# Kernel tuning notes

Hardware: AMD Instinct MI355X
Metric: run time of the kernel (lower is better)

The kernel has to match this reference:

```python
import jax, jax.numpy as jnp
import numpy as np

B = 1024        # graphs per batch
NPG = 64        # nodes per graph (uniform)
DEG = 16        # avg degree
NE_PG = 256     # candidate non-edges per graph
N = B * NPG
E = N * DEG
NE = B * NE_PG
EMB, HID, NCAT, NET, NOUT = 64, 128, 100, 4, 101  # NOUT = num_external + 1


def setup_inputs() -> dict:
    key = jax.random.key(0)
    ks = jax.random.split(key, 32)
    rn = lambda k, shape: jax.random.normal(k, shape, jnp.float32) * 0.05
    # graph structure: edges and non-edges stay within each graph's node block
    x = jax.random.randint(ks[0], (N,), 0, NCAT)
    offs = jnp.repeat(jnp.arange(B) * NPG, NPG * DEG)
    src = jax.random.randint(ks[1], (E,), 0, NPG) + offs
    dst = jax.random.randint(ks[2], (E,), 0, NPG) + offs
    edge_index = jnp.stack([src, dst])
    edge_attr = jax.random.randint(ks[3], (E,), 0, NET)
    offs_ne = jnp.repeat(jnp.arange(B) * NPG, NE_PG)
    non_edges = jax.random.randint(ks[4], (NE, 2), 0, NPG) + offs_ne[:, None]
    batch = jnp.repeat(jnp.arange(B), NPG)
    return dict(
        node_tab=rn(ks[5], (NCAT, EMB)), edge_tab=rn(ks[6], (NET, EMB)),
        c1_w=rn(ks[7], (EMB, HID)), c1_we=rn(ks[8], (EMB, HID)),
        c1_as=rn(ks[9], (HID,)), c1_ad=rn(ks[10], (HID,)), c1_ae=rn(ks[11], (HID,)), c1_b=rn(ks[12], (HID,)),
        c2_w=rn(ks[13], (HID, HID)), c2_we=rn(ks[14], (EMB, HID)),
        c2_as=rn(ks[15], (HID,)), c2_ad=rn(ks[16], (HID,)), c2_ae=rn(ks[17], (HID,)), c2_b=rn(ks[18], (HID,)),
        s_w1=rn(ks[19], (HID, HID)), s_b1=rn(ks[20], (HID,)), s_w2=rn(ks[21], (HID, 1)), s_b2=rn(ks[22], (1,)),
        n_w1=rn(ks[23], (HID, HID)), n_b1=rn(ks[24], (HID,)), n_w2=rn(ks[25], (HID, NOUT)), n_b2=rn(ks[26], (NOUT,)),
        e_w1=rn(ks[27], (HID, HID)), e_b1=rn(ks[28], (HID,)), e_w2=rn(ks[29], (HID, 1)), e_b2=rn(ks[30], (1,)),
        x=x, edge_index=edge_index, edge_attr=edge_attr, non_edges=non_edges, batch=batch,
    )


def _gat(h_in, src, dst, e, W, We, a_s, a_d, a_e, b):
    """PyG GATConv, heads=1: gather -> leakyrelu logits -> segment softmax over dst -> scatter sum."""
    n = h_in.shape[0]
    h = h_in @ W                  # [N, C]
    he = e @ We                   # [E, C]
    logit = (h @ a_s)[src] + (h @ a_d)[dst] + he @ a_e   # [E]
    logit = jnp.where(logit > 0, logit, 0.2 * logit)      # leaky_relu(0.2)
    m = jax.ops.segment_max(logit, dst, num_segments=n)
    ex = jnp.exp(logit - m[dst])
    den = jax.ops.segment_sum(ex, dst, num_segments=n)
    alpha = ex / (den[dst] + 1e-16)
    return jax.ops.segment_sum(h[src] * alpha[:, None], dst, num_segments=n) + b


def _mlp(z, w1, b1, w2, b2):
    return jax.nn.relu(z @ w1 + b1) @ w2 + b2


def reference(node_tab, edge_tab,
              c1_w, c1_we, c1_as, c1_ad, c1_ae, c1_b,
              c2_w, c2_we, c2_as, c2_ad, c2_ae, c2_b,
              s_w1, s_b1, s_w2, s_b2,
              n_w1, n_b1, n_w2, n_b2,
              e_w1, e_b1, e_w2, e_b2,
              x, edge_index, edge_attr, non_edges, batch):
    src, dst = edge_index[0], edge_index[1]
    e = edge_tab[edge_attr]                      # [E, EMB]
    h = node_tab[x]                              # [N, EMB]
    h = jax.nn.relu(_gat(h, src, dst, e, c1_w, c1_we, c1_as, c1_ad, c1_ae, c1_b))
    h = _gat(h, src, dst, e, c2_w, c2_we, c2_as, c2_ad, c2_ae, c2_b)   # [N, HID]
    g = jax.ops.segment_sum(h, batch, num_segments=B)                   # [B, HID]
    stop = _mlp(g, s_w1, s_b1, s_w2, s_b2)                              # [B, 1]
    addnode = _mlp(h, n_w1, n_b1, n_w2, n_b2)                           # [N, NOUT]
    pair = h[non_edges[:, 0]] + h[non_edges[:, 1]]                      # [NE, HID]
    addedge = _mlp(pair, e_w1, e_b1, e_w2, e_b2)                        # [NE, 1]
    # uniform per-graph sizes -> the torch split/pad is a static reshape+concat
    return jnp.concatenate(
        [stop, addnode.reshape(B, NPG * NOUT), addedge.reshape(B, NE_PG)], axis=1)
```

## Files before the change

### kernel.cpp

```cpp
#include <hip/hip_runtime.h>


#define NPG 64
#define EPG 1024
#define NEPG 256
#define B_GR 1024
#define E_TOT 1048576
#define EMB 64
#define HID 128
#define NOUT 101
#define OUT_PG 6721

typedef __attribute__((ext_vector_type(8))) short bf16x8;
typedef __attribute__((ext_vector_type(4))) float f32x4;
typedef unsigned short ushort_t;

__device__ ushort_t g_c1w[EMB*HID];
__device__ ushort_t g_c2w[HID*HID];
__device__ ushort_t g_nw1[HID*HID];
__device__ ushort_t g_ew1[HID*HID];
__device__ ushort_t g_nw2[HID*112];
__device__ float    g_sw1t[HID*HID];
__device__ float    g_he1[4], g_he2[4];

__device__ __forceinline__ ushort_t f2bf(float f) {
  unsigned u = __float_as_uint(f);
  return (ushort_t)((u + 0x7fffu + ((u >> 16) & 1u)) >> 16);
}
__device__ __forceinline__ float bf2f(ushort_t h) {
  return __uint_as_float(((unsigned)h) << 16);
}

__global__ void prep_kernel(
    const float* __restrict__ edge_tab,
    const float* __restrict__ c1_w,  const float* __restrict__ c1_we,
    const float* __restrict__ c1_ae,
    const float* __restrict__ c2_w,  const float* __restrict__ c2_we,
    const float* __restrict__ c2_ae,
    const float* __restrict__ s_w1,  const float* __restrict__ n_w1,
    const float* __restrict__ n_w2,  const float* __restrict__ e_w1)
{
  const int b = blockIdx.x, tid = threadIdx.x;
  if (b == 0) {
    __shared__ float v1[EMB], v2[EMB];
    if (tid < EMB) {
      float a = 0.f, d = 0.f;
      for (int j = 0; j < HID; ++j) {
        a = fmaf(c1_we[tid*HID + j], c1_ae[j], a);
        d = fmaf(c2_we[tid*HID + j], c2_ae[j], d);
      }
      v1[tid] = a; v2[tid] = d;
    }
    __syncthreads();
    if (tid < 4) {
      float a = 0.f, d = 0.f;
      for (int k = 0; k < EMB; ++k) {
        const float ev = edge_tab[tid*EMB + k];
        a = fmaf(ev, v1[k], a); d = fmaf(ev, v2[k], d);
      }
      g_he1[tid] = a; g_he2[tid] = d;
    }
    return;
  }
  if (b <= 4) {
    const int base = (b - 1) * 2048 + tid;
    #pragma unroll
    for (int it = 0; it < 8; ++it) {
      const int idx = base + it*256;
      const int j = idx & 7, l = (idx >> 3) & 63, r2 = idx >> 9;
      const int ks = r2 & 1, ct = r2 >> 1;
      const int row = ks*32 + (l >> 4)*8 + j;
      const int col = ct*16 + (l & 15);
      g_c1w[idx] = f2bf(c1_w[row*HID + col]);
    }
    return;
  }
  if (b <= 28) {
    const int grp = (b - 5) >> 3;
    const int chunk = (b - 5) & 7;
    const float* W = (grp == 0) ? c2_w : (grp == 1) ? n_w1 : e_w1;
    ushort_t* G = (grp == 0) ? g_c2w : (grp == 1) ? g_nw1 : g_ew1;
    const int base = chunk * 2048 + tid;
    #pragma unroll
    for (int it = 0; it < 8; ++it) {
      const int idx = base + it*256;
      const int j = idx & 7, l = (idx >> 3) & 63, r2 = idx >> 9;
      const int ks = r2 & 3, ct = r2 >> 2;
      const int row = ks*32 + (l >> 4)*8 + j;
      const int col = ct*16 + (l & 15);
      G[idx] = f2bf(W[row*HID + col]);
    }
    return;
  }
  if (b <= 35) {
    const int base = (b - 29) * 2048 + tid;
    #pragma unroll
    for (int it = 0; it < 8; ++it) {
      const int idx = base + it*256;
      const int j = idx & 7, l = (idx >> 3) & 63, r2 = idx >> 9;
      const int ks = r2 & 3, ct = r2 >> 2;
      const int row = ks*32 + (l >> 4)*8 + j;
      const int col = ct*16 + (l & 15);
      g_nw2[idx] = (col < NOUT) ? f2bf(n_w2[row*NOUT + col]) : (ushort_t)0;
    }
    return;
  }
  {
    const int base = (b - 36) * 2048 + tid;
    #pragma unroll
    for (int it = 0; it < 8; ++it) {
      const int idx = base + it*256;
      g_sw1t[idx] = s_w1[(idx & 127)*HID + (idx >> 7)];
    }
  }
}

#define S_HC   0
#define S_R    18432
#define S_PART 35840
#define S_NS   36864
#define S_ND   37120
#define S_GP   37376
#define S_EBW  37888
#define S_HCC  38912
#define S_TOT  38944

__global__ __launch_bounds__(256, 4) void graph_kernel(
    const float* __restrict__ node_tab,
    const float* __restrict__ c1_as, const float* __restrict__ c1_ad,
    const float* __restrict__ c1_b,
    const float* __restrict__ c2_as, const float* __restrict__ c2_ad,
    const float* __restrict__ c2_b,
    const float* __restrict__ s_b1,  const float* __restrict__ s_w2,
    const float* __restrict__ s_b2,
    const float* __restrict__ n_b1,  const float* __restrict__ n_b2,
    const float* __restrict__ e_b1,  const float* __restrict__ e_w2,
    const float* __restrict__ e_b2,
    const int* __restrict__ x,  const int* __restrict__ ei,
    const int* __restrict__ ea, const int* __restrict__ nedg,
    float* __restrict__ out)
{
  const int tid = threadIdx.x;
  const int gid = blockIdx.x;
  const int nb = gid * NPG;
  const int lane = tid & 63;
  const int wv = tid >> 6;
  const int qd = lane >> 4;
  const int cl = lane & 15;
  const int rb = wv * 16;

  __shared__ __align__(16) char smem[S_TOT];
  ushort_t* Hc   = (ushort_t*)(smem + S_HC);
  float*    Pf   = (float*)   (smem + S_R);
  ushort_t* Hr   = (ushort_t*)(smem + S_R);
  float*    part = (float*)   (smem + S_PART);
  float*    ns   = (float*)   (smem + S_NS);
  float*    nd   = (float*)   (smem + S_ND);
  float*    gp   = (float*)   (smem + S_GP);
  float*    ebw  = (float*)   (smem + S_EBW);
  float*    hc   = (float*)   (smem + S_HCC);
  ushort_t* a1b  = Hc;

  unsigned er[4];
  #pragma unroll
  for (int i = 0; i < 4; ++i) {
    const int k = tid + 256*i;
    const int s = ei[gid*EPG + k] - nb;
    const int d = ei[E_TOT + gid*EPG + k] - nb;
    const int t = ea[gid*EPG + k];
    er[i] = (unsigned)(s | (d << 6) | (t << 12));
  }
  const int2 prr = *(const int2*)(nedg + 2*(gid*NEPG + tid));
  bf16x8 ea0, ea1;
  {
    const int cat = x[nb + rb + cl];
    const float* src = node_tab + cat*EMB;
    const float4 v0 = *(const float4*)(src + qd*8);
    const float4 v1 = *(const float4*)(src + qd*8 + 4);
    const float4 v2 = *(const float4*)(src + 32 + qd*8);
    const float4 v3 = *(const float4*)(src + 36 + qd*8);
    ea0[0]=f2bf(v0.x); ea0[1]=f2bf(v0.y); ea0[2]=f2bf(v0.z); ea0[3]=f2bf(v0.w);
    ea0[4]=f2bf(v1.x); ea0[5]=f2bf(v1.y); ea0[6]=f2bf(v1.z); ea0[7]=f2bf(v1.w);
    ea1[0]=f2bf(v2.x); ea1[1]=f2bf(v2.y); ea1[2]=f2bf(v2.z); ea1[3]=f2bf(v2.w);
    ea1[4]=f2bf(v3.x); ea1[5]=f2bf(v3.y); ea1[6]=f2bf(v3.z); ea1[7]=f2bf(v3.w);
  }
  {
    float4* pz = (float4*)Pf;
    #pragma unroll
    for (int j = 0; j < 4; ++j) pz[tid + j*256] = make_float4(0.f,0.f,0.f,0.f);
  }
  if (tid < 128) gp[tid] = 0.f;
  ebw[tid] = (tid < 128) ? e_b1[tid] : e_w2[tid - 128];
  if (tid < 8) hc[tid] = (tid < 4) ? g_he1[tid] : g_he2[tid-4];

  {
    float pns[4] = {0.f,0.f,0.f,0.f}, pnd[4] = {0.f,0.f,0.f,0.f};
    #pragma unroll
    for (int ct = 0; ct < 8; ++ct) {
      f32x4 acc = {0.f, 0.f, 0.f, 0.f};
      const bf16x8 b0 = *(const bf16x8*)(g_c1w + ((ct*2+0)*64 + lane)*8);
      const bf16x8 b1 = *(const bf16x8*)(g_c1w + ((ct*2+1)*64 + lane)*8);
      acc = __builtin_amdgcn_mfma_f32_16x16x32_bf16(ea0, b0, acc, 0, 0, 0);
      acc = __builtin_amdgcn_mfma_f32_16x16x32_bf16(ea1, b1, acc, 0, 0, 0);
      const int n = ct*16 + cl;
      const float asv = c1_as[n], adv = c1_ad[n];
      #pragma unroll
      for (int r = 0; r < 4; ++r) {
        const float v = acc[r];
        Hc[n*72 + (rb + qd*4 + r)] = f2bf(v);
        pns[r] = fmaf(v, asv, pns[r]);
        pnd[r] = fmaf(v, adv, pnd[r]);
      }
    }
    #pragma unroll
    for (int r = 0; r < 4; ++r) {
      #pragma unroll
      for (int off = 1; off < 16; off <<= 1) {
        pns[r] += __shfl_xor(pns[r], off, 64);
        pnd[r] += __shfl_xor(pnd[r], off, 64);
      }
    }
    if (cl == 0) {
      #pragma unroll
      for (int r = 0; r < 4; ++r) { ns[rb+qd*4+r] = pns[r]; nd[rb+qd*4+r] = pnd[r]; }
    }
  }
  __syncthreads();

  #pragma unroll
  for (int i = 0; i < 4; ++i) {
    const unsigned tp = er[i];
    const int s = tp & 63, d = (tp >> 6) & 63, t = tp >> 12;
    float l = ns[s] + nd[d] + hc[t];
    l = (l > 0.f) ? l : 0.2f * l;
    atomicAdd(&Pf[d*64 + s], __expf(l));
  }
  __syncthreads();

  bf16x8 pa0, pa1;
  float inv4[4];
  {
    const float* pr = Pf + (rb + cl)*64;
    const float4 v0 = *(const float4*)(pr + qd*8);
    const float4 v1 = *(const float4*)(pr + qd*8 + 4);
    const float4 v2 = *(const float4*)(pr + 32 + qd*8);
    const float4 v3 = *(const float4*)(pr + 36 + qd*8);
    pa0[0]=f2bf(v0.x); pa0[1]=f2bf(v0.y); pa0[2]=f2bf(v0.z); pa0[3]=f2bf(v0.w);
    pa0[4]=f2bf(v1.x); pa0[5]=f2bf(v1.y); pa0[6]=f2bf(v1.z); pa0[7]=f2bf(v1.w);
    pa1[0]=f2bf(v2.x); pa1[1]=f2bf(v2.y); pa1[2]=f2bf(v2.z); pa1[3]=f2bf(v2.w);
    pa1[4]=f2bf(v3.x); pa1[5]=f2bf(v3.y); pa1[6]=f2bf(v3.z); pa1[7]=f2bf(v3.w);
    float den = v0.x+v0.y+v0.z+v0.w + v1.x+v1.y+v1.z+v1.w
              + v2.x+v2.y+v2.z+v2.w + v3.x+v3.y+v3.z+v3.w;
    den += __shfl_xor(den, 16, 64);
    den += __shfl_xor(den, 32, 64);
    #pragma unroll
    for (int r = 0; r < 4; ++r)
      inv4[r] = 1.f / (__shfl(den, qd*4 + r, 64) + 1e-16f);
  }
  __syncthreads();

  {
    #pragma unroll
    for (int ct = 0; ct < 8; ++ct) {
      f32x4 acc = {0.f, 0.f, 0.f, 0.f};
      const bf16x8 b0 = *(const bf16x8*)(Hc + (ct*16+cl)*72 + qd*8);
      const bf16x8 b1 = *(const bf16x8*)(Hc + (ct*16+cl)*72 + 32 + qd*8);
      acc = __builtin_amdgcn_mfma_f32_16x16x32_bf16(pa0, b0, acc, 0, 0, 0);
      acc = __builtin_amdgcn_mfma_f32_16x16x32_bf16(pa1, b1, acc, 0, 0, 0);
      const int n = ct*16 + cl;
      const float bias = c1_b[n];
      #pragma unroll
      for (int r = 0; r < 4; ++r)
        Hr[(rb + qd*4 + r)*136 + n] = f2bf(fmaxf(fmaf(acc[r], inv4[r], bias), 0.f));
    }
  }
  bf16x8 h1f[4];
  #pragma unroll
  for (int ks = 0; ks < 4; ++ks)
    h1f[ks] = *(const bf16x8*)(Hr + (rb+cl)*136 + ks*32 + qd*8);
  __syncthreads();

  {
    float4* pz = (float4*)Pf;
    #pragma unroll
    for (int j = 0; j < 4; ++j) pz[tid + j*256] = make_float4(0.f,0.f,0.f,0.f);
    float pns[4] = {0.f,0.f,0.f,0.f}, pnd[4] = {0.f,0.f,0.f,0.f};
    #pragma unroll
    for (int ct = 0; ct < 8; ++ct) {
      f32x4 acc = {0.f, 0.f, 0.f, 0.f};
      #pragma unroll
      for (int ks = 0; ks < 4; ++ks) {
        const bf16x8 b = *(const bf16x8*)(g_c2w + ((ct*4+ks)*64 + lane)*8);
        acc = __builtin_amdgcn_mfma_f32_16x16x32_bf16(h1f[ks], b, acc, 0, 0, 0);
      }
      const int n = ct*16 + cl;
      const float asv = c2_as[n], adv = c2_ad[n];
      #pragma unroll
      for (int r = 0; r < 4; ++r) {
        const float v = acc[r];
        Hc[n*72 + (rb + qd*4 + r)] = f2bf(v);
        pns[r] = fmaf(v, asv, pns[r]);
        pnd[r] = fmaf(v, adv, pnd[r]);
      }
    }
    #pragma unroll
    for (int r = 0; r < 4; ++r) {
      #pragma unroll
      for (int off = 1; off < 16; off <<= 1) {
        pns[r] += __shfl_xor(pns[r], off, 64);
        pnd[r] += __shfl_xor(pnd[r], off, 64);
      }
    }
    if (cl == 0) {
      #pragma unroll
      for (int r = 0; r < 4; ++r) { ns[rb+qd*4+r] = pns[r]; nd[rb+qd*4+r] = pnd[r]; }
    }
  }
  __syncthreads();

  #pragma unroll
  for (int i = 0; i < 4; ++i) {
    const unsigned tp = er[i];
    const int s = tp & 63, d = (tp >> 6) & 63, t = tp >> 12;
    float l = ns[s] + nd[d] + hc[4 + t];
    l = (l > 0.f) ? l : 0.2f * l;
    atomicAdd(&Pf[d*64 + s], __expf(l));
  }
  __syncthreads();

  {
    const float* pr = Pf + (rb + cl)*64;
    const float4 v0 = *(const float4*)(pr + qd*8);
    const float4 v1 = *(const float4*)(pr + qd*8 + 4);
    const float4 v2 = *(const float4*)(pr + 32 + qd*8);
    const float4 v3 = *(const float4*)(pr + 36 + qd*8);
    pa0[0]=f2bf(v0.x); pa0[1]=f2bf(v0.y); pa0[2]=f2bf(v0.z); pa0[3]=f2bf(v0.w);
    pa0[4]=f2bf(v1.x); pa0[5]=f2bf(v1.y); pa0[6]=f2bf(v1.z); pa0[7]=f2bf(v1.w);
    pa1[0]=f2bf(v2.x); pa1[1]=f2bf(v2.y); pa1[2]=f2bf(v2.z); pa1[3]=f2bf(v2.w);
    pa1[4]=f2bf(v3.x); pa1[5]=f2bf(v3.y); pa1[6]=f2bf(v3.z); pa1[7]=f2bf(v3.w);
    float den = v0.x+v0.y+v0.z+v0.w + v1.x+v1.y+v1.z+v1.w
              + v2.x+v2.y+v2.z+v2.w + v3.x+v3.y+v3.z+v3.w;
    den += __shfl_xor(den, 16, 64);
    den += __shfl_xor(den, 32, 64);
    #pragma unroll
    for (int r = 0; r < 4; ++r)
      inv4[r] = 1.f / (__shfl(den, qd*4 + r, 64) + 1e-16f);
  }
  __syncthreads();

  {
    #pragma unroll
    for (int ct = 0; ct < 8; ++ct) {
      f32x4 acc = {0.f, 0.f, 0.f, 0.f};
      const bf16x8 b0 = *(const bf16x8*)(Hc + (ct*16+cl)*72 + qd*8);
      const bf16x8 b1 = *(const bf16x8*)(Hc + (ct*16+cl)*72 + 32 + qd*8);
      acc = __builtin_amdgcn_mfma_f32_16x16x32_bf16(pa0, b0, acc, 0, 0, 0);
      acc = __builtin_amdgcn_mfma_f32_16x16x32_bf16(pa1, b1, acc, 0, 0, 0);
      const int n = ct*16 + cl;
      const float bias = c2_b[n];
      float colsum = 0.f;
      #pragma unroll
      for (int r = 0; r < 4; ++r) {
        const float v = fmaf(acc[r], inv4[r], bias);
        Hr[(rb + qd*4 + r)*136 + n] = f2bf(v);
        colsum += v;
      }
      colsum += __shfl_xor(colsum, 16, 64);
      colsum += __shfl_xor(colsum, 32, 64);
      if (qd == 0) atomicAdd(&gp[n], colsum);
    }
  }
  __syncthreads();

  {
    const int j = tid & 127, half = tid >> 7;
    const float* wr = g_sw1t + j*HID + half*64;
    const float* gr = gp + half*64;
    float p = 0.f;
    #pragma unroll
    for (int q = 0; q < 16; ++q) {
      const float4 w = ((const float4*)wr)[q];
      const float4 g = ((const float4*)gr)[q];
      p = fmaf(w.x, g.x, p); p = fmaf(w.y, g.y, p);
      p = fmaf(w.z, g.z, p); p = fmaf(w.w, g.w, p);
    }
    part[tid] = p;
  }
  __syncthreads();

  if (tid < 64) {
    const float z0 = fmaxf(part[tid] + part[tid+128] + s_b1[tid], 0.f);
    const float z1 = fmaxf(part[tid+64] + part[tid+192] + s_b1[tid+64], 0.f);
    float p = fmaf(z0, s_w2[tid], z1 * s_w2[tid+64]);
    #pragma unroll
    for (int off = 32; off > 0; off >>= 1) p += __shfl_down(p, off, 64);
    if (tid == 0) out[(size_t)gid*OUT_PG] = p + s_b2[0];
  }

  bf16x8 h2f[4];
  #pragma unroll
  for (int ks = 0; ks < 4; ++ks)
    h2f[ks] = *(const bf16x8*)(Hr + (rb+cl)*136 + ks*32 + qd*8);

  {
    #pragma unroll
    for (int ct = 0; ct < 8; ++ct) {
      f32x4 an = {0.f, 0.f, 0.f, 0.f};
      f32x4 ae2 = {0.f, 0.f, 0.f, 0.f};
      #pragma unroll
      for (int ks = 0; ks < 4; ++ks) {
        const bf16x8 bn = *(const bf16x8*)(g_nw1 + ((ct*4+ks)*64 + lane)*8);
        const bf16x8 be = *(const bf16x8*)(g_ew1 + ((ct*4+ks)*64 + lane)*8);
        an  = __builtin_amdgcn_mfma_f32_16x16x32_bf16(h2f[ks], bn, an, 0, 0, 0);
        ae2 = __builtin_amdgcn_mfma_f32_16x16x32_bf16(h2f[ks], be, ae2, 0, 0, 0);
      }
      const int n = ct*16 + cl;
      const float bias = n_b1[n];
      #pragma unroll
      for (int r = 0; r < 4; ++r) {
        a1b[(rb + qd*4 + r)*136 + n] = f2bf(fmaxf(an[r] + bias, 0.f));
        Hr[(rb + qd*4 + r)*136 + n] = f2bf(ae2[r]);
      }
    }
  }
  {
    bf16x8 af[4];
    #pragma unroll
    for (int ks = 0; ks < 4; ++ks)
      af[ks] = *(const bf16x8*)(a1b + (rb+cl)*136 + ks*32 + qd*8);
    float* ob = out + (size_t)gid*OUT_PG + 1;
    #pragma unroll
    for (int ct = 0; ct < 7; ++ct) {
      f32x4 acc = {0.f, 0.f, 0.f, 0.f};
      #pragma unroll
      for (int ks = 0; ks < 4; ++ks) {
        const bf16x8 b = *(const bf16x8*)(g_nw2 + ((ct*4+ks)*64 + lane)*8);
        acc = __builtin_amdgcn_mfma_f32_16x16x32_bf16(af[ks], b, acc, 0, 0, 0);
      }
      const int o = ct*16 + cl;
      if (o < NOUT) {
        const float b2 = n_b2[o];
        #pragma unroll
        for (int r = 0; r < 4; ++r)
          ob[(size_t)(rb + qd*4 + r)*NOUT + o] = acc[r] + b2;
      }
    }
  }
  __syncthreads();

  {
    const ushort_t* ui = Hr + (prr.x - nb)*136;
    const ushort_t* uj = Hr + (prr.y - nb)*136;
    float ssum = 0.f;
    #pragma unroll
    for (int q8 = 0; q8 < 16; ++q8) {
      const bf16x8 va = *(const bf16x8*)(ui + q8*8);
      const bf16x8 vb = *(const bf16x8*)(uj + q8*8);
      #pragma unroll
      for (int j = 0; j < 8; ++j) {
        const int c = q8*8 + j;
        float v = bf2f((ushort_t)va[j]) + bf2f((ushort_t)vb[j]) + ebw[c];
        v = fmaxf(v, 0.f);
        ssum = fmaf(v, ebw[128 + c], ssum);
      }
    }
    out[(size_t)gid*OUT_PG + 1 + NPG*NOUT + tid] = ssum + e_b2[0];
  }
}

extern "C" void kernel_launch(void* const* d_in, const int* in_sizes, int n_in,
                              void* d_out, int out_size, void* d_ws, size_t ws_size,
                              hipStream_t stream) {
  const float* node_tab = (const float*)d_in[0];
  const float* edge_tab = (const float*)d_in[1];
  const float* c1_w  = (const float*)d_in[2];
  const float* c1_we = (const float*)d_in[3];
  const float* c1_as = (const float*)d_in[4];
  const float* c1_ad = (const float*)d_in[5];
  const float* c1_ae = (const float*)d_in[6];
  const float* c1_b  = (const float*)d_in[7];
  const float* c2_w  = (const float*)d_in[8];
  const float* c2_we = (const float*)d_in[9];
  const float* c2_as = (const float*)d_in[10];
  const float* c2_ad = (const float*)d_in[11];
  const float* c2_ae = (const float*)d_in[12];
  const float* c2_b  = (const float*)d_in[13];
  const float* s_w1  = (const float*)d_in[14];
  const float* s_b1  = (const float*)d_in[15];
  const float* s_w2  = (const float*)d_in[16];
  const float* s_b2  = (const float*)d_in[17];
  const float* n_w1  = (const float*)d_in[18];
  const float* n_b1  = (const float*)d_in[19];
  const float* n_w2  = (const float*)d_in[20];
  const float* n_b2  = (const float*)d_in[21];
  const float* e_w1  = (const float*)d_in[22];
  const float* e_b1  = (const float*)d_in[23];
  const float* e_w2  = (const float*)d_in[24];
  const float* e_b2  = (const float*)d_in[25];
  const int* x    = (const int*)d_in[26];
  const int* ei   = (const int*)d_in[27];
  const int* ea   = (const int*)d_in[28];
  const int* nedg = (const int*)d_in[29];
  float* out = (float*)d_out;

  prep_kernel<<<dim3(44), dim3(256), 0, stream>>>(
      edge_tab, c1_w, c1_we, c1_ae, c2_w, c2_we, c2_ae,
      s_w1, n_w1, n_w2, e_w1);

  graph_kernel<<<dim3(B_GR), dim3(256), 0, stream>>>(
      node_tab, c1_as, c1_ad, c1_b, c2_as, c2_ad, c2_b,
      s_b1, s_w2, s_b2, n_b1, n_b2, e_b1, e_w2, e_b2,
      x, ei, ea, nedg, out);
}
```

Before: 190.5 us.

## Process two graphs per block to interleave independent work between barriers

Each block now handles two graphs, with per-graph shared-memory regions doubled and every phase looped over both graphs between the same barriers. The aim is more independent work per barrier (ILP), amortized loads of the shared weights and edge-bias data, and half as many blocks. In exchange, shared memory per block roughly doubles, launch bounds drop to 2 waves-per-EU hints, and register pressure rises, which cuts occupancy. With 512 blocks on 256 CUs, load balance also becomes coarser.

```diff
diff --git a/kernel.cpp b/kernel.cpp
--- a/kernel.cpp
+++ b/kernel.cpp
@@ -121,11 +121,12 @@
 #define S_NS   36864
 #define S_ND   37120
 #define S_GP   37376
-#define S_EBW  37888
-#define S_HCC  38912
-#define S_TOT  38944
-
-__global__ __launch_bounds__(256, 4) void graph_kernel(
+#define S_G    37888
+#define S_EBW  (2*S_G)
+#define S_HCC  (S_EBW + 1024)
+#define S_TOT  (S_HCC + 32)
+
+__global__ __launch_bounds__(256, 2) void graph_kernel(
     const float* __restrict__ node_tab,
     const float* __restrict__ c1_as, const float* __restrict__ c1_ad,
     const float* __restrict__ c1_b,
@@ -141,8 +142,7 @@
     float* __restrict__ out)
 {
   const int tid = threadIdx.x;
-  const int gid = blockIdx.x;
-  const int nb = gid * NPG;
+  const int g0 = blockIdx.x * 2;
   const int lane = tid & 63;
   const int wv = tid >> 6;
   const int qd = lane >> 4;
@@ -150,64 +150,74 @@
   const int rb = wv * 16;
 
   __shared__ __align__(16) char smem[S_TOT];
-  ushort_t* Hc   = (ushort_t*)(smem + S_HC);
-  float*    Pf   = (float*)   (smem + S_R);
-  ushort_t* Hr   = (ushort_t*)(smem + S_R);
-  float*    part = (float*)   (smem + S_PART);
-  float*    ns   = (float*)   (smem + S_NS);
-  float*    nd   = (float*)   (smem + S_ND);
-  float*    gp   = (float*)   (smem + S_GP);
-  float*    ebw  = (float*)   (smem + S_EBW);
-  float*    hc   = (float*)   (smem + S_HCC);
-  ushort_t* a1b  = Hc;
-
-  unsigned er[4];
-  #pragma unroll
-  for (int i = 0; i < 4; ++i) {
-    const int k = tid + 256*i;
-    const int s = ei[gid*EPG + k] - nb;
-    const int d = ei[E_TOT + gid*EPG + k] - nb;
-    const int t = ea[gid*EPG + k];
-    er[i] = (unsigned)(s | (d << 6) | (t << 12));
-  }
-  const int2 prr = *(const int2*)(nedg + 2*(gid*NEPG + tid));
-  bf16x8 ea0, ea1;
-  {
-    const int cat = x[nb + rb + cl];
+  float* ebw = (float*)(smem + S_EBW);
+  float* hc  = (float*)(smem + S_HCC);
+  ushort_t* Hc[2]; float* Pf[2]; ushort_t* Hr[2]; float* part[2];
+  float* ns[2]; float* nd[2]; float* gp[2];
+  #pragma unroll
+  for (int g = 0; g < 2; ++g) {
+    char* base = smem + g*S_G;
+    Hc[g] = (ushort_t*)(base + S_HC);
+    Pf[g] = (float*)   (base + S_R);
+    Hr[g] = (ushort_t*)(base + S_R);
+    part[g] = (float*) (base + S_PART);
+    ns[g] = (float*)   (base + S_NS);
+    nd[g] = (float*)   (base + S_ND);
+    gp[g] = (float*)   (base + S_GP);
+  }
+
+  unsigned er[2][4];
+  int2 prr[2];
+  bf16x8 ea0[2], ea1[2], pa0[2], pa1[2];
+  float inv4[2][4];
+  bf16x8 h1f[2][4], h2f[2][4];
+
+  #pragma unroll
+  for (int g = 0; g < 2; ++g) {
+    const int gg = g0 + g, nbg = gg * NPG;
+    #pragma unroll
+    for (int i = 0; i < 4; ++i) {
+      const int k = tid + 256*i;
+      const int s = ei[gg*EPG + k] - nbg;
+      const int d = ei[E_TOT + gg*EPG + k] - nbg;
+      const int t = ea[gg*EPG + k];
+      er[g][i] = (unsigned)(s | (d << 6) | (t << 12));
+    }
+    prr[g] = *(const int2*)(nedg + 2*(gg*NEPG + tid));
+    const int cat = x[nbg + rb + cl];
     const float* src = node_tab + cat*EMB;
     const float4 v0 = *(const float4*)(src + qd*8);
     const float4 v1 = *(const float4*)(src + qd*8 + 4);
     const float4 v2 = *(const float4*)(src + 32 + qd*8);
     const float4 v3 = *(const float4*)(src + 36 + qd*8);
-    ea0[0]=f2bf(v0.x); ea0[1]=f2bf(v0.y); ea0[2]=f2bf(v0.z); ea0[3]=f2bf(v0.w);
-    ea0[4]=f2bf(v1.x); ea0[5]=f2bf(v1.y); ea0[6]=f2bf(v1.z); ea0[7]=f2bf(v1.w);
-    ea1[0]=f2bf(v2.x); ea1[1]=f2bf(v2.y); ea1[2]=f2bf(v2.z); ea1[3]=f2bf(v2.w);
-    ea1[4]=f2bf(v3.x); ea1[5]=f2bf(v3.y); ea1[6]=f2bf(v3.z); ea1[7]=f2bf(v3.w);
-  }
-  {
-    float4* pz = (float4*)Pf;
+    ea0[g][0]=f2bf(v0.x); ea0[g][1]=f2bf(v0.y); ea0[g][2]=f2bf(v0.z); ea0[g][3]=f2bf(v0.w);
+    ea0[g][4]=f2bf(v1.x); ea0[g][5]=f2bf(v1.y); ea0[g][6]=f2bf(v1.z); ea0[g][7]=f2bf(v1.w);
+    ea1[g][0]=f2bf(v2.x); ea1[g][1]=f2bf(v2.y); ea1[g][2]=f2bf(v2.z); ea1[g][3]=f2bf(v2.w);
+    ea1[g][4]=f2bf(v3.x); ea1[g][5]=f2bf(v3.y); ea1[g][6]=f2bf(v3.z); ea1[g][7]=f2bf(v3.w);
+    float4* pz = (float4*)Pf[g];
     #pragma unroll
     for (int j = 0; j < 4; ++j) pz[tid + j*256] = make_float4(0.f,0.f,0.f,0.f);
-  }
-  if (tid < 128) gp[tid] = 0.f;
+    if (tid < 128) gp[g][tid] = 0.f;
+  }
   ebw[tid] = (tid < 128) ? e_b1[tid] : e_w2[tid - 128];
   if (tid < 8) hc[tid] = (tid < 4) ? g_he1[tid] : g_he2[tid-4];
 
-  {
+  #pragma unroll
+  for (int g = 0; g < 2; ++g) {
     float pns[4] = {0.f,0.f,0.f,0.f}, pnd[4] = {0.f,0.f,0.f,0.f};
     #pragma unroll
     for (int ct = 0; ct < 8; ++ct) {
       f32x4 acc = {0.f, 0.f, 0.f, 0.f};
       const bf16x8 b0 = *(const bf16x8*)(g_c1w + ((ct*2+0)*64 + lane)*8);
       const bf16x8 b1 = *(const bf16x8*)(g_c1w + ((ct*2+1)*64 + lane)*8);
-      acc = __builtin_amdgcn_mfma_f32_16x16x32_bf16(ea0, b0, acc, 0, 0, 0);
-      acc = __builtin_amdgcn_mfma_f32_16x16x32_bf16(ea1, b1, acc, 0, 0, 0);
+      acc = __builtin_amdgcn_mfma_f32_16x16x32_bf16(ea0[g], b0, acc, 0, 0, 0);
+      acc = __builtin_amdgcn_mfma_f32_16x16x32_bf16(ea1[g], b1, acc, 0, 0, 0);
       const int n = ct*16 + cl;
       const float asv = c1_as[n], adv = c1_ad[n];
       #pragma unroll
       for (int r = 0; r < 4; ++r) {
         const float v = acc[r];
-        Hc[n*72 + (rb + qd*4 + r)] = f2bf(v);
+        Hc[g][n*72 + (rb + qd*4 + r)] = f2bf(v);
         pns[r] = fmaf(v, asv, pns[r]);
         pnd[r] = fmaf(v, adv, pnd[r]);
       }
@@ -222,66 +232,69 @@
     }
     if (cl == 0) {
       #pragma unroll
-      for (int r = 0; r < 4; ++r) { ns[rb+qd*4+r] = pns[r]; nd[rb+qd*4+r] = pnd[r]; }
-    }
-  }
-  __syncthreads();
-
-  #pragma unroll
-  for (int i = 0; i < 4; ++i) {
-    const unsigned tp = er[i];
-    const int s = tp & 63, d = (tp >> 6) & 63, t = tp >> 12;
-    float l = ns[s] + nd[d] + hc[t];
-    l = (l > 0.f) ? l : 0.2f * l;
-    atomicAdd(&Pf[d*64 + s], __expf(l));
-  }
-  __syncthreads();
-
-  bf16x8 pa0, pa1;
-  float inv4[4];
-  {
-    const float* pr = Pf + (rb + cl)*64;
+      for (int r = 0; r < 4; ++r) { ns[g][rb+qd*4+r] = pns[r]; nd[g][rb+qd*4+r] = pnd[r]; }
+    }
+  }
+  __syncthreads();
+
+  #pragma unroll
+  for (int g = 0; g < 2; ++g) {
+    #pragma unroll
+    for (int i = 0; i < 4; ++i) {
+      const unsigned tp = er[g][i];
+      const int s = tp & 63, d = (tp >> 6) & 63, t = tp >> 12;
+      float l = ns[g][s] + nd[g][d] + hc[t];
+      l = (l > 0.f) ? l : 0.2f * l;
+      atomicAdd(&Pf[g][d*64 + s], __expf(l));
+    }
+  }
+  __syncthreads();
+
+  #pragma unroll
+  for (int g = 0; g < 2; ++g) {
+    const float* pr = Pf[g] + (rb + cl)*64;
     const float4 v0 = *(const float4*)(pr + qd*8);
     const float4 v1 = *(const float4*)(pr + qd*8 + 4);
     const float4 v2 = *(const float4*)(pr + 32 + qd*8);
     const float4 v3 = *(const float4*)(pr + 36 + qd*8);
-    pa0[0]=f2bf(v0.x); pa0[1]=f2bf(v0.y); pa0[2]=f2bf(v0.z); pa0[3]=f2bf(v0.w);
-    pa0[4]=f2bf(v1.x); pa0[5]=f2bf(v1.y); pa0[6]=f2bf(v1.z); pa0[7]=f2bf(v1.w);
-    pa1[0]=f2bf(v2.x); pa1[1]=f2bf(v2.y); pa1[2]=f2bf(v2.z); pa1[3]=f2bf(v2.w);
-    pa1[4]=f2bf(v3.x); pa1[5]=f2bf(v3.y); pa1[6]=f2bf(v3.z); pa1[7]=f2bf(v3.w);
+    pa0[g][0]=f2bf(v0.x); pa0[g][1]=f2bf(v0.y); pa0[g][2]=f2bf(v0.z); pa0[g][3]=f2bf(v0.w);
+    pa0[g][4]=f2bf(v1.x); pa0[g][5]=f2bf(v1.y); pa0[g][6]=f2bf(v1.z); pa0[g][7]=f2bf(v1.w);
+    pa1[g][0]=f2bf(v2.x); pa1[g][1]=f2bf(v2.y); pa1[g][2]=f2bf(v2.z); pa1[g][3]=f2bf(v2.w);
+    pa1[g][4]=f2bf(v3.x); pa1[g][5]=f2bf(v3.y); pa1[g][6]=f2bf(v3.z); pa1[g][7]=f2bf(v3.w);
     float den = v0.x+v0.y+v0.z+v0.w + v1.x+v1.y+v1.z+v1.w
               + v2.x+v2.y+v2.z+v2.w + v3.x+v3.y+v3.z+v3.w;
     den += __shfl_xor(den, 16, 64);
     den += __shfl_xor(den, 32, 64);
     #pragma unroll
     for (int r = 0; r < 4; ++r)
-      inv4[r] = 1.f / (__shfl(den, qd*4 + r, 64) + 1e-16f);
-  }
-  __syncthreads();
-
-  {
+      inv4[g][r] = 1.f / (__shfl(den, qd*4 + r, 64) + 1e-16f);
+  }
+  __syncthreads();
+
+  #pragma unroll
+  for (int g = 0; g < 2; ++g) {
     #pragma unroll
     for (int ct = 0; ct < 8; ++ct) {
       f32x4 acc = {0.f, 0.f, 0.f, 0.f};
-      const bf16x8 b0 = *(const bf16x8*)(Hc + (ct*16+cl)*72 + qd*8);
-      const bf16x8 b1 = *(const bf16x8*)(Hc + (ct*16+cl)*72 + 32 + qd*8);
-      acc = __builtin_amdgcn_mfma_f32_16x16x32_bf16(pa0, b0, acc, 0, 0, 0);
-      acc = __builtin_amdgcn_mfma_f32_16x16x32_bf16(pa1, b1, acc, 0, 0, 0);
+      const bf16x8 b0 = *(const bf16x8*)(Hc[g] + (ct*16+cl)*72 + qd*8);
+      const bf16x8 b1 = *(const bf16x8*)(Hc[g] + (ct*16+cl)*72 + 32 + qd*8);
+      acc = __builtin_amdgcn_mfma_f32_16x16x32_bf16(pa0[g], b0, acc, 0, 0, 0);
+      acc = __builtin_amdgcn_mfma_f32_16x16x32_bf16(pa1[g], b1, acc, 0, 0, 0);
       const int n = ct*16 + cl;
       const float bias = c1_b[n];
       #pragma unroll
       for (int r = 0; r < 4; ++r)
-        Hr[(rb + qd*4 + r)*136 + n] = f2bf(fmaxf(fmaf(acc[r], inv4[r], bias), 0.f));
-    }
-  }
-  bf16x8 h1f[4];
-  #pragma unroll
-  for (int ks = 0; ks < 4; ++ks)
-    h1f[ks] = *(const bf16x8*)(Hr + (rb+cl)*136 + ks*32 + qd*8);
-  __syncthreads();
-
-  {
-    float4* pz = (float4*)Pf;
+        Hr[g][(rb + qd*4 + r)*136 + n] = f2bf(fmaxf(fmaf(acc[r], inv4[g][r], bias), 0.f));
+    }
+    #pragma unroll
+    for (int ks = 0; ks < 4; ++ks)
+      h1f[g][ks] = *(const bf16x8*)(Hr[g] + (rb+cl)*136 + ks*32 + qd*8);
+  }
+  __syncthreads();
+
+  #pragma unroll
+  for (int g = 0; g < 2; ++g) {
+    float4* pz = (float4*)Pf[g];
     #pragma unroll
     for (int j = 0; j < 4; ++j) pz[tid + j*256] = make_float4(0.f,0.f,0.f,0.f);
     float pns[4] = {0.f,0.f,0.f,0.f}, pnd[4] = {0.f,0.f,0.f,0.f};
@@ -291,14 +304,14 @@
       #pragma unroll
       for (int ks = 0; ks < 4; ++ks) {
         const bf16x8 b = *(const bf16x8*)(g_c2w + ((ct*4+ks)*64 + lane)*8);
-        acc = __builtin_amdgcn_mfma_f32_16x16x32_bf16(h1f[ks], b, acc, 0, 0, 0);
+        acc = __builtin_amdgcn_mfma_f32_16x16x32_bf16(h1f[g][ks], b, acc, 0, 0, 0);
       }
       const int n = ct*16 + cl;
       const float asv = c2_as[n], adv = c2_ad[n];
       #pragma unroll
       for (int r = 0; r < 4; ++r) {
         const float v = acc[r];
-        Hc[n*72 + (rb + qd*4 + r)] = f2bf(v);
+        Hc[g][n*72 + (rb + qd*4 + r)] = f2bf(v);
         pns[r] = fmaf(v, asv, pns[r]);
         pnd[r] = fmaf(v, adv, pnd[r]);
       }
@@ -313,96 +326,101 @@
     }
     if (cl == 0) {
       #pragma unroll
-      for (int r = 0; r < 4; ++r) { ns[rb+qd*4+r] = pns[r]; nd[rb+qd*4+r] = pnd[r]; }
-    }
-  }
-  __syncthreads();
-
-  #pragma unroll
-  for (int i = 0; i < 4; ++i) {
-    const unsigned tp = er[i];
-    const int s = tp & 63, d = (tp >> 6) & 63, t = tp >> 12;
-    float l = ns[s] + nd[d] + hc[4 + t];
-    l = (l > 0.f) ? l : 0.2f * l;
-    atomicAdd(&Pf[d*64 + s], __expf(l));
-  }
-  __syncthreads();
-
-  {
-    const float* pr = Pf + (rb + cl)*64;
+      for (int r = 0; r < 4; ++r) { ns[g][rb+qd*4+r] = pns[r]; nd[g][rb+qd*4+r] = pnd[r]; }
+    }
+  }
+  __syncthreads();
+
+  #pragma unroll
+  for (int g = 0; g < 2; ++g) {
+    #pragma unroll
+    for (int i = 0; i < 4; ++i) {
+      const unsigned tp = er[g][i];
+      const int s = tp & 63, d = (tp >> 6) & 63, t = tp >> 12;
+      float l = ns[g][s] + nd[g][d] + hc[4 + t];
+      l = (l > 0.f) ? l : 0.2f * l;
+      atomicAdd(&Pf[g][d*64 + s], __expf(l));
+    }
+  }
+  __syncthreads();
+
+  #pragma unroll
+  for (int g = 0; g < 2; ++g) {
+    const float* pr = Pf[g] + (rb + cl)*64;
     const float4 v0 = *(const float4*)(pr + qd*8);
     const float4 v1 = *(const float4*)(pr + qd*8 + 4);
     const float4 v2 = *(const float4*)(pr + 32 + qd*8);
     const float4 v3 = *(const float4*)(pr + 36 + qd*8);
-    pa0[0]=f2bf(v0.x); pa0[1]=f2bf(v0.y); pa0[2]=f2bf(v0.z); pa0[3]=f2bf(v0.w);
-    pa0[4]=f2bf(v1.x); pa0[5]=f2bf(v1.y); pa0[6]=f2bf(v1.z); pa0[7]=f2bf(v1.w);
-    pa1[0]=f2bf(v2.x); pa1[1]=f2bf(v2.y); pa1[2]=f2bf(v2.z); pa1[3]=f2bf(v2.w);
-    pa1[4]=f2bf(v3.x); pa1[5]=f2bf(v3.y); pa1[6]=f2bf(v3.z); pa1[7]=f2bf(v3.w);
+    pa0[g][0]=f2bf(v0.x); pa0[g][1]=f2bf(v0.y); pa0[g][2]=f2bf(v0.z); pa0[g][3]=f2bf(v0.w);
+    pa0[g][4]=f2bf(v1.x); pa0[g][5]=f2bf(v1.y); pa0[g][6]=f2bf(v1.z); pa0[g][7]=f2bf(v1.w);
+    pa1[g][0]=f2bf(v2.x); pa1[g][1]=f2bf(v2.y); pa1[g][2]=f2bf(v2.z); pa1[g][3]=f2bf(v2.w);
+    pa1[g][4]=f2bf(v3.x); pa1[g][5]=f2bf(v3.y); pa1[g][6]=f2bf(v3.z); pa1[g][7]=f2bf(v3.w);
     float den = v0.x+v0.y+v0.z+v0.w + v1.x+v1.y+v1.z+v1.w
               + v2.x+v2.y+v2.z+v2.w + v3.x+v3.y+v3.z+v3.w;
     den += __shfl_xor(den, 16, 64);
     den += __shfl_xor(den, 32, 64);
     #pragma unroll
     for (int r = 0; r < 4; ++r)
-      inv4[r] = 1.f / (__shfl(den, qd*4 + r, 64) + 1e-16f);
-  }
-  __syncthreads();
-
-  {
+      inv4[g][r] = 1.f / (__shfl(den, qd*4 + r, 64) + 1e-16f);
+  }
+  __syncthreads();
+
+  #pragma unroll
+  for (int g = 0; g < 2; ++g) {
     #pragma unroll
     for (int ct = 0; ct < 8; ++ct) {
       f32x4 acc = {0.f, 0.f, 0.f, 0.f};
-      const bf16x8 b0 = *(const bf16x8*)(Hc + (ct*16+cl)*72 + qd*8);
-      const bf16x8 b1 = *(const bf16x8*)(Hc + (ct*16+cl)*72 + 32 + qd*8);
-      acc = __builtin_amdgcn_mfma_f32_16x16x32_bf16(pa0, b0, acc, 0, 0, 0);
-      acc = __builtin_amdgcn_mfma_f32_16x16x32_bf16(pa1, b1, acc, 0, 0, 0);
+      const bf16x8 b0 = *(const bf16x8*)(Hc[g] + (ct*16+cl)*72 + qd*8);
+      const bf16x8 b1 = *(const bf16x8*)(Hc[g] + (ct*16+cl)*72 + 32 + qd*8);
+      acc = __builtin_amdgcn_mfma_f32_16x16x32_bf16(pa0[g], b0, acc, 0, 0, 0);
+      acc = __builtin_amdgcn_mfma_f32_16x16x32_bf16(pa1[g], b1, acc, 0, 0, 0);
       const int n = ct*16 + cl;
       const float bias = c2_b[n];
       float colsum = 0.f;
       #pragma unroll
       for (int r = 0; r < 4; ++r) {
-        const float v = fmaf(acc[r], inv4[r], bias);
-        Hr[(rb + qd*4 + r)*136 + n] = f2bf(v);
+        const float v = fmaf(acc[r], inv4[g][r], bias);
+        Hr[g][(rb + qd*4 + r)*136 + n] = f2bf(v);
         colsum += v;
       }
       colsum += __shfl_xor(colsum, 16, 64);
       colsum += __shfl_xor(colsum, 32, 64);
-      if (qd == 0) atomicAdd(&gp[n], colsum);
-    }
-  }
-  __syncthreads();
-
-  {
+      if (qd == 0) atomicAdd(&gp[g][n], colsum);
+    }
+  }
+  __syncthreads();
+
+  #pragma unroll
+  for (int g = 0; g < 2; ++g) {
     const int j = tid & 127, half = tid >> 7;
     const float* wr = g_sw1t + j*HID + half*64;
-    const float* gr = gp + half*64;
+    const float* gr = gp[g] + half*64;
     float p = 0.f;
     #pragma unroll
     for (int q = 0; q < 16; ++q) {
       const float4 w = ((const float4*)wr)[q];
-      const float4 g = ((const float4*)gr)[q];
-      p = fmaf(w.x, g.x, p); p = fmaf(w.y, g.y, p);
-      p = fmaf(w.z, g.z, p); p = fmaf(w.w, g.w, p);
-    }
-    part[tid] = p;
-  }
-  __syncthreads();
-
-  if (tid < 64) {
-    const float z0 = fmaxf(part[tid] + part[tid+128] + s_b1[tid], 0.f);
-    const float z1 = fmaxf(part[tid+64] + part[tid+192] + s_b1[tid+64], 0.f);
-    float p = fmaf(z0, s_w2[tid], z1 * s_w2[tid+64]);
-    #pragma unroll
-    for (int off = 32; off > 0; off >>= 1) p += __shfl_down(p, off, 64);
-    if (tid == 0) out[(size_t)gid*OUT_PG] = p + s_b2[0];
-  }
-
-  bf16x8 h2f[4];
-  #pragma unroll
-  for (int ks = 0; ks < 4; ++ks)
-    h2f[ks] = *(const bf16x8*)(Hr + (rb+cl)*136 + ks*32 + qd*8);
-
-  {
+      const float4 gv = ((const float4*)gr)[q];
+      p = fmaf(w.x, gv.x, p); p = fmaf(w.y, gv.y, p);
+      p = fmaf(w.z, gv.z, p); p = fmaf(w.w, gv.w, p);
+    }
+    part[g][tid] = p;
+  }
+  __syncthreads();
+
+  #pragma unroll
+  for (int g = 0; g < 2; ++g) {
+    const int gg = g0 + g;
+    if (tid < 64) {
+      const float z0 = fmaxf(part[g][tid] + part[g][tid+128] + s_b1[tid], 0.f);
+      const float z1 = fmaxf(part[g][tid+64] + part[g][tid+192] + s_b1[tid+64], 0.f);
+      float p = fmaf(z0, s_w2[tid], z1 * s_w2[tid+64]);
+      #pragma unroll
+      for (int off = 32; off > 0; off >>= 1) p += __shfl_down(p, off, 64);
+      if (tid == 0) out[(size_t)gg*OUT_PG] = p + s_b2[0];
+    }
+    #pragma unroll
+    for (int ks = 0; ks < 4; ++ks)
+      h2f[g][ks] = *(const bf16x8*)(Hr[g] + (rb+cl)*136 + ks*32 + qd*8);
     #pragma unroll
     for (int ct = 0; ct < 8; ++ct) {
       f32x4 an = {0.f, 0.f, 0.f, 0.f};
@@ -411,24 +429,22 @@
       for (int ks = 0; ks < 4; ++ks) {
         const bf16x8 bn = *(const bf16x8*)(g_nw1 + ((ct*4+ks)*64 + lane)*8);
         const bf16x8 be = *(const bf16x8*)(g_ew1 + ((ct*4+ks)*64 + lane)*8);
-        an  = __builtin_amdgcn_mfma_f32_16x16x32_bf16(h2f[ks], bn, an, 0, 0, 0);
-        ae2 = __builtin_amdgcn_mfma_f32_16x16x32_bf16(h2f[ks], be, ae2, 0, 0, 0);
+        an  = __builtin_amdgcn_mfma_f32_16x16x32_bf16(h2f[g][ks], bn, an, 0, 0, 0);
+        ae2 = __builtin_amdgcn_mfma_f32_16x16x32_bf16(h2f[g][ks], be, ae2, 0, 0, 0);
       }
       const int n = ct*16 + cl;
       const float bias = n_b1[n];
       #pragma unroll
       for (int r = 0; r < 4; ++r) {
-        a1b[(rb + qd*4 + r)*136 + n] = f2bf(fmaxf(an[r] + bias, 0.f));
-        Hr[(rb + qd*4 + r)*136 + n] = f2bf(ae2[r]);
-      }
-    }
-  }
-  {
+        Hc[g][(rb + qd*4 + r)*136 + n] = f2bf(fmaxf(an[r] + bias, 0.f));
+        Hr[g][(rb + qd*4 + r)*136 + n] = f2bf(ae2[r]);
+      }
+    }
     bf16x8 af[4];
     #pragma unroll
     for (int ks = 0; ks < 4; ++ks)
-      af[ks] = *(const bf16x8*)(a1b + (rb+cl)*136 + ks*32 + qd*8);
-    float* ob = out + (size_t)gid*OUT_PG + 1;
+      af[ks] = *(const bf16x8*)(Hc[g] + (rb+cl)*136 + ks*32 + qd*8);
+    float* ob = out + (size_t)gg*OUT_PG + 1;
     #pragma unroll
     for (int ct = 0; ct < 7; ++ct) {
       f32x4 acc = {0.f, 0.f, 0.f, 0.f};
@@ -448,9 +464,11 @@
   }
   __syncthreads();
 
-  {
-    const ushort_t* ui = Hr + (prr.x - nb)*136;
-    const ushort_t* uj = Hr + (prr.y - nb)*136;
+  #pragma unroll
+  for (int g = 0; g < 2; ++g) {
+    const int gg = g0 + g, nbg = gg * NPG;
+    const ushort_t* ui = Hr[g] + (prr[g].x - nbg)*136;
+    const ushort_t* uj = Hr[g] + (prr[g].y - nbg)*136;
     float ssum = 0.f;
     #pragma unroll
     for (int q8 = 0; q8 < 16; ++q8) {
@@ -464,7 +482,7 @@
         ssum = fmaf(v, ebw[128 + c], ssum);
       }
     }
-    out[(size_t)gid*OUT_PG + 1 + NPG*NOUT + tid] = ssum + e_b2[0];
+    out[(size_t)gg*OUT_PG + 1 + NPG*NOUT + tid] = ssum + e_b2[0];
   }
 }
 
@@ -507,7 +525,7 @@
       edge_tab, c1_w, c1_we, c1_ae, c2_w, c2_we, c2_ae,
       s_w1, n_w1, n_w2, e_w1);
 
-  graph_kernel<<<dim3(B_GR), dim3(256), 0, stream>>>(
+  graph_kernel<<<dim3(B_GR/2), dim3(256), 0, stream>>>(
       node_tab, c1_as, c1_ad, c1_b, c2_as, c2_ad, c2_b,
       s_b1, s_w2, s_b2, n_b1, n_b2, e_b1, e_w2, e_b2,
       x, ei, ea, nedg, out);
```

Result: slower. 251.8 us (+32.2%).
